# Kernel tuning notes

Measured on AMD Instinct MI355X. Metric: run time of the kernel, lower is better.

The kernel has to match this reference:

```python
import jax, jax.numpy as jnp
import numpy as np

B, N, F, R = 8, 1024, 512, 32


def setup_inputs() -> dict:
    key = jax.random.key(0)
    kx, k1, k2, kg = jax.random.split(key, 4)
    scale = 0.02  # keep activations moderate (glorot-ish)
    return {
        "x": jax.random.normal(kx, (B, N, F), dtype=jnp.float32),
        "W1": jax.random.normal(k1, (F, R), dtype=jnp.float32) * scale,
        "W2": jax.random.normal(k2, (F, R), dtype=jnp.float32) * scale,
        "Wg": jax.random.normal(kg, (F, R), dtype=jnp.float32) * scale,
        "b": jnp.zeros((R,), dtype=jnp.float32),
    }


def reference(x, W1, W2, Wg, b):
    # Original math:
    #   z1[b,i,r] = (x @ W1 + bias)[b,i,r]
    #   z2[b,j,r] = (x @ W2)[b,j,r]
    #   g[b,j,r]  = (x @ Wg)[b,j,r]
    #   out[b,i,r] = sum_j (z1[b,i,r] + z2[b,j,r]) * g[b,j,r]
    # Algebraically identical fused form (avoids the [B,N,N,R] intermediate):
    #   out = z1 * sum_j g  +  sum_j (z2 * g)
    z1 = jnp.einsum("bnf,fr->bnr", x, W1) + b          # [B,N,R]
    z2 = jnp.einsum("bnf,fr->bnr", x, W2)              # [B,N,R]
    g = jnp.einsum("bnf,fr->bnr", x, Wg)               # [B,N,R]
    g_sum = jnp.sum(g, axis=1, keepdims=True)           # [B,1,R]
    z2g_sum = jnp.sum(z2 * g, axis=1, keepdims=True)    # [B,1,R]
    return z1 * g_sum + z2g_sum                          # [B,N,R]
```

## Files before the change

kernel.cpp:

```cpp
#include <hip/hip_runtime.h>

#define Bn 8
#define Nn 1024
#define Fn 512
#define Rn 32

#define T1   512
#define ROWS 32
#define GR   (T1 / Rn)
#define RPT  (ROWS / GR)

__global__ __launch_bounds__(T1)
void k1(const float* __restrict__ x, const float* __restrict__ W1,
        const float* __restrict__ W2, const float* __restrict__ Wg,
        const float* __restrict__ bias, float* __restrict__ z1out,
        float* __restrict__ gsum, float* __restrict__ z2gsum)
{
    __shared__ float xs[ROWS * Fn];
    const int t = threadIdx.x;
    const int row0 = blockIdx.x * ROWS;
    const int bb = row0 / Nn;

    {
        float4* s4 = (float4*)xs;
        const float4* g4 = (const float4*)(x + (size_t)row0 * Fn);
        #pragma unroll
        for (int i = 0; i < (ROWS * Fn / 4) / T1; ++i)
            s4[t + i * T1] = g4[t + i * T1];
    }
    __syncthreads();

    const int r = t & (Rn - 1);
    const int g = t >> 5;

    float a1[RPT] = {0.f, 0.f};
    float a2[RPT] = {0.f, 0.f};
    float ag[RPT] = {0.f, 0.f};
    const float4* xr0 = (const float4*)(xs + (g * RPT + 0) * Fn);
    const float4* xr1 = (const float4*)(xs + (g * RPT + 1) * Fn);
    const float* w1p = W1 + r;
    const float* w2p = W2 + r;
    const float* wgp = Wg + r;

    #pragma unroll 4
    for (int f4 = 0; f4 < Fn / 4; ++f4) {
        float4 v0 = xr0[f4];
        float4 v1 = xr1[f4];
        float xv[RPT][4] = {{v0.x, v0.y, v0.z, v0.w},
                            {v1.x, v1.y, v1.z, v1.w}};
        #pragma unroll
        for (int k = 0; k < 4; ++k) {
            const int f = f4 * 4 + k;
            const float w1 = w1p[f * Rn];
            const float w2 = w2p[f * Rn];
            const float wg = wgp[f * Rn];
            #pragma unroll
            for (int i = 0; i < RPT; ++i) {
                a1[i] = fmaf(xv[i][k], w1, a1[i]);
                a2[i] = fmaf(xv[i][k], w2, a2[i]);
                ag[i] = fmaf(xv[i][k], wg, ag[i]);
            }
        }
    }

    const float bv = bias[r];
    if (z1out) {
        #pragma unroll
        for (int i = 0; i < RPT; ++i)
            z1out[(size_t)(row0 + g * RPT + i) * Rn + r] = a1[i] + bv;
    }

    float pg = 0.f, pz = 0.f;
    #pragma unroll
    for (int i = 0; i < RPT; ++i) { pg += ag[i]; pz += a2[i] * ag[i]; }

    __syncthreads();
    xs[g * Rn + r]            = pg;
    xs[GR * Rn + g * Rn + r]  = pz;
    __syncthreads();
    if (t < Rn) {
        float sg = 0.f, sz = 0.f;
        #pragma unroll
        for (int gg = 0; gg < GR; ++gg) {
            sg += xs[gg * Rn + t];
            sz += xs[GR * Rn + gg * Rn + t];
        }
        atomicAdd(&gsum[bb * Rn + t], sg);
        atomicAdd(&z2gsum[bb * Rn + t], sz);
    }
}

__global__ __launch_bounds__(256)
void k2(const float4* __restrict__ z1, const float* __restrict__ gsum,
        const float* __restrict__ z2gsum, float4* __restrict__ out)
{
    const int i = blockIdx.x * 256 + threadIdx.x;
    const int e = i << 2;
    const int bb = e >> 15;
    const int rb = e & (Rn - 1);
    const float4 z  = z1[i];
    const float4 gs = *(const float4*)(gsum   + bb * Rn + rb);
    const float4 zg = *(const float4*)(z2gsum + bb * Rn + rb);
    float4 o;
    o.x = fmaf(z.x, gs.x, zg.x);
    o.y = fmaf(z.y, gs.y, zg.y);
    o.z = fmaf(z.z, gs.z, zg.z);
    o.w = fmaf(z.w, gs.w, zg.w);
    out[i] = o;
}

__global__ __launch_bounds__(T1)
void k2b(const float* __restrict__ x, const float* __restrict__ W1,
         const float* __restrict__ bias, const float* __restrict__ gsum,
         const float* __restrict__ z2gsum, float* __restrict__ out)
{
    __shared__ float xs[ROWS * Fn];
    const int t = threadIdx.x;
    const int row0 = blockIdx.x * ROWS;
    const int bb = row0 / Nn;

    {
        float4* s4 = (float4*)xs;
        const float4* g4 = (const float4*)(x + (size_t)row0 * Fn);
        #pragma unroll
        for (int i = 0; i < (ROWS * Fn / 4) / T1; ++i)
            s4[t + i * T1] = g4[t + i * T1];
    }
    __syncthreads();

    const int r = t & (Rn - 1);
    const int g = t >> 5;
    float a1[RPT] = {0.f, 0.f};
    const float4* xr0 = (const float4*)(xs + (g * RPT + 0) * Fn);
    const float4* xr1 = (const float4*)(xs + (g * RPT + 1) * Fn);
    const float* w1p = W1 + r;

    #pragma unroll 4
    for (int f4 = 0; f4 < Fn / 4; ++f4) {
        float4 v0 = xr0[f4];
        float4 v1 = xr1[f4];
        float xv[RPT][4] = {{v0.x, v0.y, v0.z, v0.w},
                            {v1.x, v1.y, v1.z, v1.w}};
        #pragma unroll
        for (int k = 0; k < 4; ++k) {
            const float w1 = w1p[(f4 * 4 + k) * Rn];
            #pragma unroll
            for (int i = 0; i < RPT; ++i)
                a1[i] = fmaf(xv[i][k], w1, a1[i]);
        }
    }

    const float gv0 = gsum[bb * Rn + r];
    const float zg0 = z2gsum[bb * Rn + r];
    const float bv  = bias[r];
    #pragma unroll
    for (int i = 0; i < RPT; ++i) {
        const int row = row0 + g * RPT + i;
        out[(size_t)row * Rn + r] = fmaf(a1[i] + bv, gv0, zg0);
    }
}

extern "C" void kernel_launch(void* const* d_in, const int* in_sizes, int n_in,
                              void* d_out, int out_size, void* d_ws, size_t ws_size,
                              hipStream_t stream)
{
    const float* x    = (const float*)d_in[0];
    const float* W1   = (const float*)d_in[1];
    const float* W2   = (const float*)d_in[2];
    const float* Wg   = (const float*)d_in[3];
    const float* bias = (const float*)d_in[4];
    float* out = (float*)d_out;

    const size_t z1_bytes  = (size_t)Bn * Nn * Rn * sizeof(float);
    const size_t sum_bytes = (size_t)2 * Bn * Rn * sizeof(float);
    const bool big = ws_size >= z1_bytes + sum_bytes;

    float* z1     = big ? (float*)d_ws : nullptr;
    float* gsum   = big ? (float*)((char*)d_ws + z1_bytes) : (float*)d_ws;
    float* z2gsum = gsum + Bn * Rn;

    hipMemsetAsync(gsum, 0, sum_bytes, stream);

    k1<<<dim3((Bn * Nn) / ROWS), dim3(T1), 0, stream>>>(
        x, W1, W2, Wg, bias, z1, gsum, z2gsum);

    if (big) {
        k2<<<dim3((Bn * Nn * Rn / 4) / 256), dim3(256), 0, stream>>>(
            (const float4*)z1, gsum, z2gsum, (float4*)out);
    } else {
        k2b<<<dim3((Bn * Nn) / ROWS), dim3(T1), 0, stream>>>(
            x, W1, bias, gsum, z2gsum, out);
    }
}
```

Baseline: 99.61 us.

## Compute projections with bf16 MFMA using pre-transposed bf16 weights

Adds a small kernel that transposes W1/W2/Wg into a bf16 [R,F] layout in the workspace. The main kernel now uses 64-thread blocks that each handle 16 rows, converting x to bf16 on the fly and accumulating the three projections with 16x16x32 bf16 MFMA instructions instead of scalar FP32 FMAs from LDS. The block reduction moves from LDS to wave shuffles, and the fallback path for a small workspace is removed. This trades FP32 precision for bf16 inputs, which may loosen accuracy against the reference, and it assumes the workspace is large enough.

```diff
diff --git a/kernel.cpp b/kernel.cpp
--- a/kernel.cpp
+++ b/kernel.cpp
@@ -1,92 +1,110 @@
 #include <hip/hip_runtime.h>
+#include <hip/hip_bf16.h>
 
 #define Bn 8
 #define Nn 1024
 #define Fn 512
 #define Rn 32
 
-#define T1   512
-#define ROWS 32
-#define GR   (T1 / Rn)
-#define RPT  (ROWS / GR)
+typedef __attribute__((ext_vector_type(8))) short bf16x8;
+typedef __attribute__((ext_vector_type(4))) float f32x4;
 
-__global__ __launch_bounds__(T1)
-void k1(const float* __restrict__ x, const float* __restrict__ W1,
-        const float* __restrict__ W2, const float* __restrict__ Wg,
-        const float* __restrict__ bias, float* __restrict__ z1out,
-        float* __restrict__ gsum, float* __restrict__ z2gsum)
+__global__ __launch_bounds__(256)
+void kW(const float* __restrict__ W1, const float* __restrict__ W2,
+        const float* __restrict__ Wg, short* __restrict__ Wt)
 {
-    __shared__ float xs[ROWS * Fn];
+    __shared__ float xs[64 * 33];
+    const int m  = blockIdx.x >> 3;
+    const int f0 = (blockIdx.x & 7) * 64;
+    const float* W = (m == 0) ? W1 : (m == 1) ? W2 : Wg;
     const int t = threadIdx.x;
-    const int row0 = blockIdx.x * ROWS;
-    const int bb = row0 / Nn;
 
-    {
-        float4* s4 = (float4*)xs;
-        const float4* g4 = (const float4*)(x + (size_t)row0 * Fn);
-        #pragma unroll
-        for (int i = 0; i < (ROWS * Fn / 4) / T1; ++i)
-            s4[t + i * T1] = g4[t + i * T1];
+    #pragma unroll
+    for (int i = 0; i < 8; ++i) {
+        int idx = t + i * 256;
+        int fi = idx >> 5, r = idx & 31;
+        xs[fi * 33 + r] = W[(size_t)(f0 + fi) * Rn + r];
     }
     __syncthreads();
 
-    const int r = t & (Rn - 1);
-    const int g = t >> 5;
+    short* out = Wt + (size_t)m * (Rn * Fn);
+    #pragma unroll
+    for (int i = 0; i < 8; ++i) {
+        int j = t + i * 256;
+        int r = j >> 6, fi = j & 63;
+        __hip_bfloat16 h = __float2bfloat16(xs[fi * 33 + r]);
+        out[(size_t)r * Fn + f0 + fi] = *reinterpret_cast<short*>(&h);
+    }
+}
 
-    float a1[RPT] = {0.f, 0.f};
-    float a2[RPT] = {0.f, 0.f};
-    float ag[RPT] = {0.f, 0.f};
-    const float4* xr0 = (const float4*)(xs + (g * RPT + 0) * Fn);
-    const float4* xr1 = (const float4*)(xs + (g * RPT + 1) * Fn);
-    const float* w1p = W1 + r;
-    const float* w2p = W2 + r;
-    const float* wgp = Wg + r;
+__global__ __launch_bounds__(64)
+void k1(const float* __restrict__ x, const short* __restrict__ Wt,
+        const float* __restrict__ bias, float* __restrict__ z1,
+        float* __restrict__ gsum, float* __restrict__ z2gsum)
+{
+    const int l    = threadIdx.x;
+    const int row0 = blockIdx.x * 16;
+    const int bb   = row0 >> 10;
+    const int lr   = l & 15;
+    const int lk   = l >> 4;
 
-    #pragma unroll 4
-    for (int f4 = 0; f4 < Fn / 4; ++f4) {
-        float4 v0 = xr0[f4];
-        float4 v1 = xr1[f4];
-        float xv[RPT][4] = {{v0.x, v0.y, v0.z, v0.w},
-                            {v1.x, v1.y, v1.z, v1.w}};
+    const float* xrow = x + (size_t)(row0 + lr) * Fn + 8 * lk;
+    const short* w0   = Wt + 8 * lk;
+
+    f32x4 acc1[2] = {}, acc2[2] = {}, accg[2] = {};
+
+    #pragma unroll
+    for (int kk = 0; kk < 16; ++kk) {
+        float4 v0 = *(const float4*)(xrow + kk * 32);
+        float4 v1 = *(const float4*)(xrow + kk * 32 + 4);
+        float f[8] = {v0.x, v0.y, v0.z, v0.w, v1.x, v1.y, v1.z, v1.w};
+        bf16x8 a;
         #pragma unroll
-        for (int k = 0; k < 4; ++k) {
-            const int f = f4 * 4 + k;
-            const float w1 = w1p[f * Rn];
-            const float w2 = w2p[f * Rn];
-            const float wg = wgp[f * Rn];
-            #pragma unroll
-            for (int i = 0; i < RPT; ++i) {
-                a1[i] = fmaf(xv[i][k], w1, a1[i]);
-                a2[i] = fmaf(xv[i][k], w2, a2[i]);
-                ag[i] = fmaf(xv[i][k], wg, ag[i]);
-            }
+        for (int i = 0; i < 8; ++i) {
+            __hip_bfloat16 h = __float2bfloat16(f[i]);
+            a[i] = *reinterpret_cast<short*>(&h);
+        }
+        #pragma unroll
+        for (int h = 0; h < 2; ++h) {
+            const short* wp = w0 + (size_t)(h * 16 + lr) * Fn + kk * 32;
+            bf16x8 b1 = *(const bf16x8*)(wp);
+            bf16x8 b2 = *(const bf16x8*)(wp + 16384);
+            bf16x8 bg = *(const bf16x8*)(wp + 32768);
+            acc1[h] = __builtin_amdgcn_mfma_f32_16x16x32_bf16(a, b1, acc1[h], 0, 0, 0);
+            acc2[h] = __builtin_amdgcn_mfma_f32_16x16x32_bf16(a, b2, acc2[h], 0, 0, 0);
+            accg[h] = __builtin_amdgcn_mfma_f32_16x16x32_bf16(a, bg, accg[h], 0, 0, 0);
         }
     }
 
-    const float bv = bias[r];
-    if (z1out) {
+    const float bv[2] = {bias[lr], bias[16 + lr]};
+    #pragma unroll
+    for (int h = 0; h < 2; ++h) {
         #pragma unroll
-        for (int i = 0; i < RPT; ++i)
-            z1out[(size_t)(row0 + g * RPT + i) * Rn + r] = a1[i] + bv;
+        for (int reg = 0; reg < 4; ++reg) {
+            int row = row0 + lk * 4 + reg;
+            z1[(size_t)row * Rn + h * 16 + lr] = acc1[h][reg] + bv[h];
+        }
     }
 
-    float pg = 0.f, pz = 0.f;
+    float sg[2] = {0.f, 0.f}, sz[2] = {0.f, 0.f};
     #pragma unroll
-    for (int i = 0; i < RPT; ++i) { pg += ag[i]; pz += a2[i] * ag[i]; }
-
-    __syncthreads();
-    xs[g * Rn + r]            = pg;
-    xs[GR * Rn + g * Rn + r]  = pz;
-    __syncthreads();
-    if (t < Rn) {
-        float sg = 0.f, sz = 0.f;
+    for (int h = 0; h < 2; ++h)
         #pragma unroll
-        for (int gg = 0; gg < GR; ++gg) {
-            sg += xs[gg * Rn + t];
-            sz += xs[GR * Rn + gg * Rn + t];
+        for (int reg = 0; reg < 4; ++reg) {
+            float gv = accg[h][reg];
+            sg[h] += gv;
+            sz[h] += acc2[h][reg] * gv;
         }
-        atomicAdd(&gsum[bb * Rn + t], sg);
-        atomicAdd(&z2gsum[bb * Rn + t], sz);
+    #pragma unroll
+    for (int h = 0; h < 2; ++h) {
+        sg[h] += __shfl_xor(sg[h], 16); sg[h] += __shfl_xor(sg[h], 32);
+        sz[h] += __shfl_xor(sz[h], 16); sz[h] += __shfl_xor(sz[h], 32);
+    }
+    if (l < 16) {
+        atomicAdd(&gsum[bb * Rn + lr],        sg[0]);
+        atomicAdd(&gsum[bb * Rn + 16 + lr],   sg[1]);
+        atomicAdd(&z2gsum[bb * Rn + lr],      sz[0]);
+        atomicAdd(&z2gsum[bb * Rn + 16 + lr], sz[1]);
     }
 }
 
@@ -109,57 +127,6 @@
     out[i] = o;
 }
 
-__global__ __launch_bounds__(T1)
-void k2b(const float* __restrict__ x, const float* __restrict__ W1,
-         const float* __restrict__ bias, const float* __restrict__ gsum,
-         const float* __restrict__ z2gsum, float* __restrict__ out)
-{
-    __shared__ float xs[ROWS * Fn];
-    const int t = threadIdx.x;
-    const int row0 = blockIdx.x * ROWS;
-    const int bb = row0 / Nn;
-
-    {
-        float4* s4 = (float4*)xs;
-        const float4* g4 = (const float4*)(x + (size_t)row0 * Fn);
-        #pragma unroll
-        for (int i = 0; i < (ROWS * Fn / 4) / T1; ++i)
-            s4[t + i * T1] = g4[t + i * T1];
-    }
-    __syncthreads();
-
-    const int r = t & (Rn - 1);
-    const int g = t >> 5;
-    float a1[RPT] = {0.f, 0.f};
-    const float4* xr0 = (const float4*)(xs + (g * RPT + 0) * Fn);
-    const float4* xr1 = (const float4*)(xs + (g * RPT + 1) * Fn);
-    const float* w1p = W1 + r;
-
-    #pragma unroll 4
-    for (int f4 = 0; f4 < Fn / 4; ++f4) {
-        float4 v0 = xr0[f4];
-        float4 v1 = xr1[f4];
-        float xv[RPT][4] = {{v0.x, v0.y, v0.z, v0.w},
-                            {v1.x, v1.y, v1.z, v1.w}};
-        #pragma unroll
-        for (int k = 0; k < 4; ++k) {
-            const float w1 = w1p[(f4 * 4 + k) * Rn];
-            #pragma unroll
-            for (int i = 0; i < RPT; ++i)
-                a1[i] = fmaf(xv[i][k], w1, a1[i]);
-        }
-    }
-
-    const float gv0 = gsum[bb * Rn + r];
-    const float zg0 = z2gsum[bb * Rn + r];
-    const float bv  = bias[r];
-    #pragma unroll
-    for (int i = 0; i < RPT; ++i) {
-        const int row = row0 + g * RPT + i;
-        out[(size_t)row * Rn + r] = fmaf(a1[i] + bv, gv0, zg0);
-    }
-}
-
 extern "C" void kernel_launch(void* const* d_in, const int* in_sizes, int n_in,
                               void* d_out, int out_size, void* d_ws, size_t ws_size,
                               hipStream_t stream)
@@ -171,24 +138,18 @@
     const float* bias = (const float*)d_in[4];
     float* out = (float*)d_out;
 
-    const size_t z1_bytes  = (size_t)Bn * Nn * Rn * sizeof(float);
-    const size_t sum_bytes = (size_t)2 * Bn * Rn * sizeof(float);
-    const bool big = ws_size >= z1_bytes + sum_bytes;
-
-    float* z1     = big ? (float*)d_ws : nullptr;
-    float* gsum   = big ? (float*)((char*)d_ws + z1_bytes) : (float*)d_ws;
+    short* Wt     = (short*)d_ws;
+    float* z1     = (float*)((char*)d_ws + 3 * Rn * Fn * sizeof(short));
+    float* gsum   = (float*)((char*)z1 + (size_t)Bn * Nn * Rn * sizeof(float));
     float* z2gsum = gsum + Bn * Rn;
 
-    hipMemsetAsync(gsum, 0, sum_bytes, stream);
+    hipMemsetAsync(gsum, 0, 2 * Bn * Rn * sizeof(float), stream);
 
-    k1<<<dim3((Bn * Nn) / ROWS), dim3(T1), 0, stream>>>(
-        x, W1, W2, Wg, bias, z1, gsum, z2gsum);
+    kW<<<dim3(24), dim3(256), 0, stream>>>(W1, W2, Wg, Wt);
 
-    if (big) {
-        k2<<<dim3((Bn * Nn * Rn / 4) / 256), dim3(256), 0, stream>>>(
-            (const float4*)z1, gsum, z2gsum, (float4*)out);
-    } else {
-        k2b<<<dim3((Bn * Nn) / ROWS), dim3(T1), 0, stream>>>(
-            x, W1, bias, gsum, z2gsum, out);
-    }
+    k1<<<dim3((Bn * Nn) / 16), dim3(64), 0, stream>>>(
+        x, Wt, bias, z1, gsum, z2gsum);
+
+    k2<<<dim3((Bn * Nn * Rn / 4) / 256), dim3(256), 0, stream>>>(
+        (const float4*)z1, gsum, z2gsum, (float4*)out);
 }
```

After: 83.38 us. 1.19x faster.
